# Kernel optimization log

Hardware: AMD Instinct MI355X
Metric: run time of the kernel (lower is better)

## Reference

```python
import jax, jax.numpy as jnp
import numpy as np

NUM_HEADS = 8
NUM_GROUPS = 32
EPS = 1e-5


def group_norm(x, gamma, beta):
    b, c, h, w = x.shape
    xg = x.reshape(b, NUM_GROUPS, c // NUM_GROUPS, h, w)
    mean = jnp.mean(xg, axis=(2, 3, 4), keepdims=True)
    var = jnp.var(xg, axis=(2, 3, 4), keepdims=True)
    xn = ((xg - mean) * jax.lax.rsqrt(var + EPS)).reshape(b, c, h, w)
    return xn * gamma[None, :, None, None] + beta[None, :, None, None]


def setup_inputs() -> dict:
    key = jax.random.key(0)
    ks = jax.random.split(key, 4)
    b, c, h, w = 16, 512, 32, 32
    x = jax.random.normal(ks[0], (b, c, h, w), dtype=jnp.float32)
    gn_gamma = jnp.ones((c,), dtype=jnp.float32)
    gn_beta = jnp.zeros((c,), dtype=jnp.float32)
    qkv_w = jax.random.normal(ks[1], (3 * c, c), dtype=jnp.float32) * (1.0 / np.sqrt(c))
    qkv_b = jnp.zeros((3 * c,), dtype=jnp.float32)
    proj_w = jax.random.normal(ks[2], (c, c), dtype=jnp.float32) * (1.0 / np.sqrt(c))
    proj_b = jnp.zeros((c,), dtype=jnp.float32)
    return {"x": x, "gn_gamma": gn_gamma, "gn_beta": gn_beta,
            "qkv_w": qkv_w, "qkv_b": qkv_b, "proj_w": proj_w, "proj_b": proj_b}


def reference(x, gn_gamma, gn_beta, qkv_w, qkv_b, proj_w, proj_b):
    b, c, h, w = x.shape
    hd = c // NUM_HEADS
    hw = h * w

    xn = group_norm(x, gn_gamma, gn_beta)
    # 1x1 conv == channel matmul
    qkv = jnp.einsum('oc,bchw->bohw', qkv_w, xn) + qkv_b[None, :, None, None]
    q, k, v = jnp.split(qkv, 3, axis=1)
    q = q.reshape(b, NUM_HEADS, hd, hw)
    k = k.reshape(b, NUM_HEADS, hd, hw)
    v = v.reshape(b, NUM_HEADS, hd, hw)

    scale = 1.0 / np.sqrt(hd)
    attn = jnp.einsum('bhdt,bhds->bhts', q, k) * scale  # [b,H,hw,hw]
    attn = jax.nn.softmax(attn, axis=-1)
    h_attn = jnp.einsum('bhts,bhds->bhdt', attn, v).reshape(b, c, h, w)

    h_attn = jnp.einsum('oc,bchw->bohw', proj_w, h_attn) + proj_b[None, :, None, None]
    return x + h_attn
```

## Files before the change

kernel.cpp:

```cpp
#include <hip/hip_runtime.h>
#include <math.h>

#define NUM_HEADS 8
#define NUM_GROUPS 32
#define EPS 1e-5f

constexpr int B  = 16;
constexpr int C  = 512;
constexpr int HW = 1024;
constexpr int HD = 64;

typedef short bf16x8 __attribute__((ext_vector_type(8)));
typedef float f32x4  __attribute__((ext_vector_type(4)));

#define QSCALE 0.1803368801111f

__device__ inline unsigned short f2bf(float f) {
    union { float f; unsigned int u; } v; v.f = f;
    unsigned int r = (v.u + 0x7FFFu + ((v.u >> 16) & 1u)) >> 16;
    return (unsigned short)r;
}

__device__ __forceinline__ unsigned int pack_trunc(float lo, float hi) {
    return __builtin_amdgcn_perm(__float_as_uint(hi), __float_as_uint(lo), 0x07060302u);
}

__device__ __forceinline__ void gld_lds16(void* lds, const void* g) {
    __builtin_amdgcn_global_load_lds(
        (const __attribute__((address_space(1))) void*)g,
        (__attribute__((address_space(3))) void*)lds, 16, 0, 0);
}

__global__ __launch_bounds__(256)
void groupnorm_t_kernel(const float* __restrict__ x,
                        const float* __restrict__ gamma,
                        const float* __restrict__ beta,
                        unsigned short* __restrict__ xnT) {
    const int bg = blockIdx.x;
    const int b = bg >> 5, g = bg & 31;
    const size_t base = ((size_t)b * C + (size_t)g * 16) * HW;

    float v[4][16];
    float sum = 0.f, sumsq = 0.f;
    #pragma unroll
    for (int p = 0; p < 4; ++p) {
        const int t = threadIdx.x + p * 256;
        #pragma unroll
        for (int cl = 0; cl < 16; ++cl) {
            const float f = x[base + (size_t)cl * HW + t];
            v[p][cl] = f;
            sum += f;
            sumsq += f * f;
        }
    }
    #pragma unroll
    for (int off = 32; off > 0; off >>= 1) {
        sum   += __shfl_down(sum, off, 64);
        sumsq += __shfl_down(sumsq, off, 64);
    }
    __shared__ float s_sum[4], s_sq[4];
    const int wid = threadIdx.x >> 6, lane = threadIdx.x & 63;
    if (lane == 0) { s_sum[wid] = sum; s_sq[wid] = sumsq; }
    __syncthreads();
    const float tsum = s_sum[0] + s_sum[1] + s_sum[2] + s_sum[3];
    const float tsq  = s_sq[0] + s_sq[1] + s_sq[2] + s_sq[3];
    const float mean = tsum * (1.0f / 16384.f);
    const float var  = tsq * (1.0f / 16384.f) - mean * mean;
    const float rstd = rsqrtf(var + EPS);

    float ga[16], be[16];
    #pragma unroll
    for (int cl = 0; cl < 16; ++cl) {
        ga[cl] = gamma[g * 16 + cl] * rstd;
        be[cl] = beta[g * 16 + cl] - mean * ga[cl];
    }

    #pragma unroll
    for (int p = 0; p < 4; ++p) {
        const int t = threadIdx.x + p * 256;
        unsigned short pk[16];
        #pragma unroll
        for (int cl = 0; cl < 16; ++cl)
            pk[cl] = f2bf(v[p][cl] * ga[cl] + be[cl]);
        unsigned short* dst = xnT + ((size_t)(b * 1024 + t)) * 512 + g * 16;
        *(uint4*)dst = *(const uint4*)pk;
        *(uint4*)(dst + 8) = *(const uint4*)(pk + 8);
    }
}

__global__ __launch_bounds__(256)
void wconv_kernel(const float* __restrict__ qkv_w,
                  const float* __restrict__ proj_w,
                  unsigned short* __restrict__ wqb) {
    const int i = blockIdx.x * 256 + threadIdx.x;
    const int n1 = 786432 / 4;
    const int nt = 1048576 / 4;
    if (i >= nt) return;
    const float4 v = (i < n1) ? ((const float4*)qkv_w)[i]
                              : ((const float4*)proj_w)[i - n1];
    ushort4 r;
    r.x = f2bf(v.x); r.y = f2bf(v.y); r.z = f2bf(v.z); r.w = f2bf(v.w);
    ((ushort4*)wqb)[i] = r;
}

__device__ __forceinline__ void mfma_gemm_core(const char* __restrict__ Ab,
                                               const char* __restrict__ Bb,
                                               unsigned short* As,
                                               unsigned short* Bs,
                                               f32x4 acc[4][4]) {
    const int tid = threadIdx.x;
    const int w = tid >> 6, lane = tid & 63;
    const int lo = lane & 15, q4 = lane >> 4;
    const int wm = w >> 1, wn = w & 1;
    const int lrow = lane >> 2, lkc = lane & 3;

    for (int k0 = 0; k0 < 512; k0 += 32) {
        __syncthreads();
        #pragma unroll
        for (int i = 0; i < 2; ++i) {
            const int row = w * 32 + i * 16 + lrow;
            const int kc = lkc ^ ((row >> 1) & 3);
            const size_t goff = (size_t)row * 1024 + k0 * 2 + kc * 16;
            gld_lds16((char*)As + w * 2048 + i * 1024, Ab + goff);
            gld_lds16((char*)Bs + w * 2048 + i * 1024, Bb + goff);
        }
        __syncthreads();

        bf16x8 af[4], bfr[4];
        #pragma unroll
        for (int i = 0; i < 4; ++i) {
            const int ra = wm * 64 + i * 16 + lo;
            af[i]  = *(const bf16x8*)(As + ra * 32 + (q4 ^ ((ra >> 1) & 3)) * 8);
            const int rb = wn * 64 + i * 16 + lo;
            bfr[i] = *(const bf16x8*)(Bs + rb * 32 + (q4 ^ ((rb >> 1) & 3)) * 8);
        }
        #pragma unroll
        for (int mi = 0; mi < 4; ++mi)
            #pragma unroll
            for (int ni = 0; ni < 4; ++ni)
                acc[mi][ni] = __builtin_amdgcn_mfma_f32_16x16x32_bf16(
                    af[mi], bfr[ni], acc[mi][ni], 0, 0, 0);
    }
}

__global__ __launch_bounds__(256)
void qkv_mfma_kernel(const unsigned short* __restrict__ wqb,
                     const unsigned short* __restrict__ xnT,
                     const float* __restrict__ qkv_b,
                     unsigned short* __restrict__ Qt,
                     unsigned short* __restrict__ Kt,
                     unsigned short* __restrict__ Vb) {
    __shared__ __align__(16) unsigned short SMEM[8192];
    unsigned short* As = SMEM;
    unsigned short* Bs = SMEM + 4096;
    const int batch = blockIdx.z;
    const int mBase = blockIdx.y * 128, nBase = blockIdx.x * 128;

    f32x4 acc[4][4] = {};
    mfma_gemm_core((const char*)(wqb + (size_t)mBase * 512),
                   (const char*)(xnT + ((size_t)batch * 1024 + nBase) * 512),
                   As, Bs, acc);

    const int tid = threadIdx.x;
    const int w = tid >> 6, lane = tid & 63;
    const int lo = lane & 15, q4 = lane >> 4;
    const int wm = w >> 1, wn = w & 1;
    const int mw = mBase + wm * 64;
    const int tb = nBase + wn * 64;

    __syncthreads();

    if (mw < 1024) {
        const bool isQ = mw < 512;
        const int head = (mw >> 6) & 7;
        unsigned short* dst = (isQ ? Qt : Kt) + (((size_t)batch * 8 + head) << 16);
        const float sc = isQ ? QSCALE : 1.0f;
        #pragma unroll
        for (int mi = 0; mi < 4; ++mi) {
            const float4 bq = *(const float4*)(qkv_b + mw + mi * 16 + q4 * 4);
            #pragma unroll
            for (int ni = 0; ni < 4; ++ni) {
                const int t = tb + ni * 16 + lo;
                ushort4 pk;
                pk.x = f2bf((acc[mi][ni][0] + bq.x) * sc);
                pk.y = f2bf((acc[mi][ni][1] + bq.y) * sc);
                pk.z = f2bf((acc[mi][ni][2] + bq.z) * sc);
                pk.w = f2bf((acc[mi][ni][3] + bq.w) * sc);
                *(ushort4*)(dst + (size_t)t * 64 + mi * 16 + q4 * 4) = pk;
            }
        }
    } else {
        unsigned short* T = SMEM + w * 2048;
        unsigned short* Vrow = Vb + (size_t)batch * 524288 + (size_t)(mw - 1024) * 1024 + tb;
        const int rl8 = lane >> 3, c8 = lane & 7;
        #pragma unroll
        for (int p = 0; p < 2; ++p) {
            #pragma unroll
            for (int mi2 = 0; mi2 < 2; ++mi2) {
                const int mi = 2 * p + mi2;
                const float4 bq = *(const float4*)(qkv_b + mw + mi * 16 + q4 * 4);
                const int dl = mi2 * 16 + q4 * 4;
                #pragma unroll
                for (int ni = 0; ni < 4; ++ni) {
                    const int tl = ni * 16 + lo;
                    T[(dl + 0) * 64 + tl] = f2bf(acc[mi][ni][0] + bq.x);
                    T[(dl + 1) * 64 + tl] = f2bf(acc[mi][ni][1] + bq.y);
                    T[(dl + 2) * 64 + tl] = f2bf(acc[mi][ni][2] + bq.z);
                    T[(dl + 3) * 64 + tl] = f2bf(acc[mi][ni][3] + bq.w);
                }
            }
            #pragma unroll
            for (int i = 0; i < 4; ++i) {
                const int dl = i * 8 + rl8;
                const uint4 val = *(const uint4*)&T[dl * 64 + c8 * 8];
                *(uint4*)(Vrow + (size_t)(p * 32 + dl) * 1024 + c8 * 8) = val;
            }
        }
    }
}

__global__ __launch_bounds__(256, 2)
void attn_mfma_kernel(const unsigned short* __restrict__ Qt,
                      const unsigned short* __restrict__ Kt,
                      const unsigned short* __restrict__ Vb,
                      unsigned short* __restrict__ attnT) {
    const int bh = blockIdx.x;
    const int b = bh >> 3, h = bh & 7;
    const int tBase = blockIdx.y * 256;
    const int tid = threadIdx.x;
    const int w = tid >> 6, lane = tid & 63;
    const int lo = lane & 15, q4 = lane >> 4;
    const int xr = lo & 7;

    __shared__ __align__(16) unsigned short Ks[2][64 * 64];
    __shared__ __align__(16) unsigned short Vs[2][64 * 64];
    __shared__ __align__(16) unsigned short Ps[4][64 * 64];

    const unsigned short* Kp = Kt + ((size_t)bh << 16);
    const unsigned short* Vp = Vb + ((size_t)b * 512 + h * 64) * 1024;

    bf16x8 qf[4][2];
    {
        const unsigned short* Qp = Qt + ((size_t)bh * 1024 + tBase + 64 * w) * 64;
        #pragma unroll
        for (int nt = 0; nt < 4; ++nt) {
            qf[nt][0] = *(const bf16x8*)(Qp + (size_t)(16 * nt + lo) * 64 + 8 * q4);
            qf[nt][1] = *(const bf16x8*)(Qp + (size_t)(16 * nt + lo) * 64 + 32 + 8 * q4);
        }
    }

    const int rl = lane >> 3, p8 = lane & 7;
    auto stage = [&](unsigned short* Kd, unsigned short* Vd, int s0) {
        #pragma unroll
        for (int cc = 0; cc < 2; ++cc) {
            const int r = 16 * w + 8 * cc + rl;
            const int j = p8 ^ (r & 7);
            gld_lds16(Kd + (16 * w + 8 * cc) * 64, Kp + (size_t)(s0 + r) * 64 + j * 8);
            gld_lds16(Vd + (16 * w + 8 * cc) * 64, Vp + (size_t)r * 1024 + s0 + j * 8);
        }
    };

    f32x4 oacc[4][4] = {};
    float lrun[4] = {0.f, 0.f, 0.f, 0.f};
    unsigned short* Pw = Ps[w];

    stage(Ks[0], Vs[0], 0);

    for (int i = 0; i < 16; ++i) {
        __syncthreads();
        if (i < 15) stage(Ks[(i + 1) & 1], Vs[(i + 1) & 1], (i + 1) * 64);
        const unsigned short* Kcur = Ks[i & 1];
        const unsigned short* Vcur = Vs[i & 1];

        f32x4 sacc[4][4] = {};
        #pragma unroll
        for (int mt = 0; mt < 4; ++mt) {
            const unsigned short* kr = Kcur + (16 * mt + lo) * 64;
            const bf16x8 a0 = *(const bf16x8*)(kr + ((q4    ) ^ xr) * 8);
            const bf16x8 a1 = *(const bf16x8*)(kr + ((q4 + 4) ^ xr) * 8);
            #pragma unroll
            for (int nt = 0; nt < 4; ++nt) {
                sacc[mt][nt] = __builtin_amdgcn_mfma_f32_16x16x32_bf16(a0, qf[nt][0], sacc[mt][nt], 0, 0, 0);
                sacc[mt][nt] = __builtin_amdgcn_mfma_f32_16x16x32_bf16(a1, qf[nt][1], sacc[mt][nt], 0, 0, 0);
            }
        }

        #pragma unroll
        for (int nt = 0; nt < 4; ++nt) {
            float ps = 0.f;
            const int t = 16 * nt + lo;
            #pragma unroll
            for (int mt = 0; mt < 4; ++mt) {
                const f32x4 s = sacc[mt][nt];
                const float p0 = exp2f(s[0]);
                const float p1 = exp2f(s[1]);
                const float p2 = exp2f(s[2]);
                const float p3 = exp2f(s[3]);
                ps += (p0 + p1) + (p2 + p3);
                uint2 pk;
                pk.x = pack_trunc(p0, p1);
                pk.y = pack_trunc(p2, p3);
                const int sc = 2 * mt + (q4 >> 1);
                *(uint2*)(Pw + t * 64 + ((sc ^ xr) * 8) + 4 * (q4 & 1)) = pk;
            }
            lrun[nt] += ps;
        }

        bf16x8 bp[4][2];
        #pragma unroll
        for (int nt = 0; nt < 4; ++nt) {
            const unsigned short* pr = Pw + (16 * nt + lo) * 64;
            bp[nt][0] = *(const bf16x8*)(pr + ((q4    ) ^ xr) * 8);
            bp[nt][1] = *(const bf16x8*)(pr + ((q4 + 4) ^ xr) * 8);
        }
        #pragma unroll
        for (int mt = 0; mt < 4; ++mt) {
            const unsigned short* vr = Vcur + (16 * mt + lo) * 64;
            const bf16x8 v0 = *(const bf16x8*)(vr + ((q4    ) ^ xr) * 8);
            const bf16x8 v1 = *(const bf16x8*)(vr + ((q4 + 4) ^ xr) * 8);
            #pragma unroll
            for (int nt = 0; nt < 4; ++nt) {
                oacc[mt][nt] = __builtin_amdgcn_mfma_f32_16x16x32_bf16(v0, bp[nt][0], oacc[mt][nt], 0, 0, 0);
                oacc[mt][nt] = __builtin_amdgcn_mfma_f32_16x16x32_bf16(v1, bp[nt][1], oacc[mt][nt], 0, 0, 0);
            }
        }
    }

    #pragma unroll
    for (int nt = 0; nt < 4; ++nt) {
        float lt = lrun[nt];
        lt += __shfl_xor(lt, 16, 64);
        lt += __shfl_xor(lt, 32, 64);
        const float inv = 1.0f / lt;
        const int t = tBase + 64 * w + 16 * nt + lo;
        unsigned short* op = attnT + ((size_t)(b * 1024 + t)) * 512 + h * 64;
        #pragma unroll
        for (int mt = 0; mt < 4; ++mt) {
            uint2 pk;
            pk.x = pack_trunc(oacc[mt][nt][0] * inv, oacc[mt][nt][1] * inv);
            pk.y = pack_trunc(oacc[mt][nt][2] * inv, oacc[mt][nt][3] * inv);
            *(uint2*)(op + 16 * mt + 4 * q4) = pk;
        }
    }
}

__global__ __launch_bounds__(256)
void proj_mfma_kernel(const unsigned short* __restrict__ wpb,
                      const unsigned short* __restrict__ attnT,
                      const float* __restrict__ proj_b,
                      const float* __restrict__ x,
                      float* __restrict__ out) {
    __shared__ __align__(16) unsigned short As[128 * 32];
    __shared__ __align__(16) unsigned short Bs[128 * 32];
    const int batch = blockIdx.z;
    const int mBase = blockIdx.y * 128, nBase = blockIdx.x * 128;

    f32x4 acc[4][4] = {};
    mfma_gemm_core((const char*)(wpb + (size_t)mBase * 512),
                   (const char*)(attnT + ((size_t)batch * 1024 + nBase) * 512),
                   As, Bs, acc);

    const int tid = threadIdx.x;
    const int w = tid >> 6, lane = tid & 63;
    const int lo = lane & 15, q4 = lane >> 4;
    const int wm = w >> 1, wn = w & 1;
    const float* xb = x + (size_t)batch * 524288;
    float* ob = out + (size_t)batch * 524288;

    #pragma unroll
    for (int mi = 0; mi < 4; ++mi) {
        const int m0 = mBase + wm * 64 + mi * 16 + q4 * 4;
        const float4 bq = *(const float4*)(proj_b + m0);
        #pragma unroll
        for (int ni = 0; ni < 4; ++ni) {
            const int t = nBase + wn * 64 + ni * 16 + lo;
            const size_t o0 = (size_t)m0 * 1024 + t;
            ob[o0]          = acc[mi][ni][0] + bq.x + xb[o0];
            ob[o0 + 1024]   = acc[mi][ni][1] + bq.y + xb[o0 + 1024];
            ob[o0 + 2048]   = acc[mi][ni][2] + bq.z + xb[o0 + 2048];
            ob[o0 + 3072]   = acc[mi][ni][3] + bq.w + xb[o0 + 3072];
        }
    }
}

extern "C" void kernel_launch(void* const* d_in, const int* in_sizes, int n_in,
                              void* d_out, int out_size, void* d_ws, size_t ws_size,
                              hipStream_t stream) {
    const float* x        = (const float*)d_in[0];
    const float* gn_gamma = (const float*)d_in[1];
    const float* gn_beta  = (const float*)d_in[2];
    const float* qkv_w    = (const float*)d_in[3];
    const float* qkv_b    = (const float*)d_in[4];
    const float* proj_w   = (const float*)d_in[5];
    const float* proj_b   = (const float*)d_in[6];
    float* out = (float*)d_out;

    char* wsc = (char*)d_ws;
    unsigned short* xnT   = (unsigned short*)(wsc);
    unsigned short* Qt    = (unsigned short*)(wsc + 16777216);
    unsigned short* Kt    = (unsigned short*)(wsc + 33554432);
    unsigned short* Vb    = (unsigned short*)(wsc + 50331648);
    unsigned short* attnT = (unsigned short*)(wsc + 67108864);
    unsigned short* wqb   = (unsigned short*)(wsc + 83886080);
    unsigned short* wpb   = wqb + 786432;

    groupnorm_t_kernel<<<B * NUM_GROUPS, 256, 0, stream>>>(x, gn_gamma, gn_beta, xnT);

    wconv_kernel<<<1024, 256, 0, stream>>>(qkv_w, proj_w, wqb);

    {
        dim3 grid(HW / 128, (3 * C) / 128, B);
        qkv_mfma_kernel<<<grid, 256, 0, stream>>>(wqb, xnT, qkv_b, Qt, Kt, Vb);
    }

    {
        dim3 grid(B * NUM_HEADS, HW / 256);
        attn_mfma_kernel<<<grid, 256, 0, stream>>>(Qt, Kt, Vb, attnT);
    }

    {
        dim3 grid(HW / 128, C / 128, B);
        proj_mfma_kernel<<<grid, 256, 0, stream>>>(wpb, attnT, proj_b, x, out);
    }
}
```

Measured before the change: 239.0 us.

## Split attention over key halves with combine kernel and XCD-aware block mapping

The attention kernel now splits the key/value sequence into two halves per block, doubling the grid to 1024 blocks. Blocks are remapped so each XCD handles contiguous heads for L2 reuse. A new combine kernel merges the partial outputs and row sums. The K/V tiles are no longer double buffered, so loads are not overlapped with compute, and the PV multiply is split into two phases to reduce register pressure, allowing three blocks per CU. This adds a bf16 round trip of partial outputs through global memory plus an extra launch.

```diff
diff --git a/kernel.cpp b/kernel.cpp
--- a/kernel.cpp
+++ b/kernel.cpp
@@ -219,22 +219,28 @@
     }
 }
 
-__global__ __launch_bounds__(256, 2)
+__global__ __launch_bounds__(256, 3)
 void attn_mfma_kernel(const unsigned short* __restrict__ Qt,
                       const unsigned short* __restrict__ Kt,
                       const unsigned short* __restrict__ Vb,
-                      unsigned short* __restrict__ attnT) {
-    const int bh = blockIdx.x;
+                      unsigned short* __restrict__ Opart,
+                      float* __restrict__ lpart) {
+    const int blk = blockIdx.x;
+    const int cxd = blk & 7, j = blk >> 3;
+    const int bh = cxd * 16 + (j >> 3);
+    const int ts = j & 7;
+    const int tt = ts >> 1, sh = ts & 1;
     const int b = bh >> 3, h = bh & 7;
-    const int tBase = blockIdx.y * 256;
+    const int tBase = tt * 256;
+    const int sBase = sh * 512;
     const int tid = threadIdx.x;
     const int w = tid >> 6, lane = tid & 63;
     const int lo = lane & 15, q4 = lane >> 4;
     const int xr = lo & 7;
 
-    __shared__ __align__(16) unsigned short Ks[2][64 * 64];
-    __shared__ __align__(16) unsigned short Vs[2][64 * 64];
-    __shared__ __align__(16) unsigned short Ps[4][64 * 64];
+    __shared__ __align__(16) unsigned short Ks[64 * 64];
+    __shared__ __align__(16) unsigned short Vs[64 * 64];
+    __shared__ __align__(16) unsigned short Ps[4 * 4096];
 
     const unsigned short* Kp = Kt + ((size_t)bh << 16);
     const unsigned short* Vp = Vb + ((size_t)b * 512 + h * 64) * 1024;
@@ -250,98 +256,119 @@
     }
 
     const int rl = lane >> 3, p8 = lane & 7;
-    auto stage = [&](unsigned short* Kd, unsigned short* Vd, int s0) {
+    auto stage = [&](int s0) {
         #pragma unroll
         for (int cc = 0; cc < 2; ++cc) {
             const int r = 16 * w + 8 * cc + rl;
-            const int j = p8 ^ (r & 7);
-            gld_lds16(Kd + (16 * w + 8 * cc) * 64, Kp + (size_t)(s0 + r) * 64 + j * 8);
-            gld_lds16(Vd + (16 * w + 8 * cc) * 64, Vp + (size_t)r * 1024 + s0 + j * 8);
+            const int jj = p8 ^ (r & 7);
+            gld_lds16(Ks + (16 * w + 8 * cc) * 64, Kp + (size_t)(s0 + r) * 64 + jj * 8);
+            gld_lds16(Vs + (16 * w + 8 * cc) * 64, Vp + (size_t)r * 1024 + s0 + jj * 8);
         }
     };
 
     f32x4 oacc[4][4] = {};
     float lrun[4] = {0.f, 0.f, 0.f, 0.f};
-    unsigned short* Pw = Ps[w];
-
-    stage(Ks[0], Vs[0], 0);
-
-    for (int i = 0; i < 16; ++i) {
+    unsigned short* Pw = Ps + w * 4096;
+
+    for (int i = 0; i < 8; ++i) {
+        if (i) __syncthreads();
+        stage(sBase + i * 64);
         __syncthreads();
-        if (i < 15) stage(Ks[(i + 1) & 1], Vs[(i + 1) & 1], (i + 1) * 64);
-        const unsigned short* Kcur = Ks[i & 1];
-        const unsigned short* Vcur = Vs[i & 1];
-
-        f32x4 sacc[4][4] = {};
-        #pragma unroll
-        for (int mt = 0; mt < 4; ++mt) {
-            const unsigned short* kr = Kcur + (16 * mt + lo) * 64;
-            const bf16x8 a0 = *(const bf16x8*)(kr + ((q4    ) ^ xr) * 8);
-            const bf16x8 a1 = *(const bf16x8*)(kr + ((q4 + 4) ^ xr) * 8);
+        #pragma unroll
+        for (int ph = 0; ph < 2; ++ph) {
+            f32x4 sacc[2][4] = {};
+            #pragma unroll
+            for (int ml = 0; ml < 2; ++ml) {
+                const unsigned short* kr = Ks + (16 * (2 * ph + ml) + lo) * 64;
+                const bf16x8 a0 = *(const bf16x8*)(kr + ((q4    ) ^ xr) * 8);
+                const bf16x8 a1 = *(const bf16x8*)(kr + ((q4 + 4) ^ xr) * 8);
+                #pragma unroll
+                for (int nt = 0; nt < 4; ++nt) {
+                    sacc[ml][nt] = __builtin_amdgcn_mfma_f32_16x16x32_bf16(a0, qf[nt][0], sacc[ml][nt], 0, 0, 0);
+                    sacc[ml][nt] = __builtin_amdgcn_mfma_f32_16x16x32_bf16(a1, qf[nt][1], sacc[ml][nt], 0, 0, 0);
+                }
+            }
             #pragma unroll
             for (int nt = 0; nt < 4; ++nt) {
-                sacc[mt][nt] = __builtin_amdgcn_mfma_f32_16x16x32_bf16(a0, qf[nt][0], sacc[mt][nt], 0, 0, 0);
-                sacc[mt][nt] = __builtin_amdgcn_mfma_f32_16x16x32_bf16(a1, qf[nt][1], sacc[mt][nt], 0, 0, 0);
-            }
-        }
-
-        #pragma unroll
-        for (int nt = 0; nt < 4; ++nt) {
-            float ps = 0.f;
-            const int t = 16 * nt + lo;
-            #pragma unroll
-            for (int mt = 0; mt < 4; ++mt) {
-                const f32x4 s = sacc[mt][nt];
-                const float p0 = exp2f(s[0]);
-                const float p1 = exp2f(s[1]);
-                const float p2 = exp2f(s[2]);
-                const float p3 = exp2f(s[3]);
-                ps += (p0 + p1) + (p2 + p3);
-                uint2 pk;
-                pk.x = pack_trunc(p0, p1);
-                pk.y = pack_trunc(p2, p3);
-                const int sc = 2 * mt + (q4 >> 1);
-                *(uint2*)(Pw + t * 64 + ((sc ^ xr) * 8) + 4 * (q4 & 1)) = pk;
-            }
-            lrun[nt] += ps;
-        }
-
-        bf16x8 bp[4][2];
-        #pragma unroll
-        for (int nt = 0; nt < 4; ++nt) {
-            const unsigned short* pr = Pw + (16 * nt + lo) * 64;
-            bp[nt][0] = *(const bf16x8*)(pr + ((q4    ) ^ xr) * 8);
-            bp[nt][1] = *(const bf16x8*)(pr + ((q4 + 4) ^ xr) * 8);
-        }
-        #pragma unroll
-        for (int mt = 0; mt < 4; ++mt) {
-            const unsigned short* vr = Vcur + (16 * mt + lo) * 64;
-            const bf16x8 v0 = *(const bf16x8*)(vr + ((q4    ) ^ xr) * 8);
-            const bf16x8 v1 = *(const bf16x8*)(vr + ((q4 + 4) ^ xr) * 8);
-            #pragma unroll
-            for (int nt = 0; nt < 4; ++nt) {
-                oacc[mt][nt] = __builtin_amdgcn_mfma_f32_16x16x32_bf16(v0, bp[nt][0], oacc[mt][nt], 0, 0, 0);
-                oacc[mt][nt] = __builtin_amdgcn_mfma_f32_16x16x32_bf16(v1, bp[nt][1], oacc[mt][nt], 0, 0, 0);
-            }
-        }
-    }
-
+                const int t = 16 * nt + lo;
+                float ps = 0.f;
+                #pragma unroll
+                for (int ml = 0; ml < 2; ++ml) {
+                    const f32x4 s = sacc[ml][nt];
+                    const float p0 = exp2f(s[0]);
+                    const float p1 = exp2f(s[1]);
+                    const float p2 = exp2f(s[2]);
+                    const float p3 = exp2f(s[3]);
+                    ps += (p0 + p1) + (p2 + p3);
+                    uint2 pk;
+                    pk.x = pack_trunc(p0, p1);
+                    pk.y = pack_trunc(p2, p3);
+                    const int sc = 4 * ph + 2 * ml + (q4 >> 1);
+                    *(uint2*)(Pw + t * 64 + ((sc ^ xr) * 8) + 4 * (q4 & 1)) = pk;
+                }
+                lrun[nt] += ps;
+            }
+            bf16x8 bp[4];
+            #pragma unroll
+            for (int nt = 0; nt < 4; ++nt)
+                bp[nt] = *(const bf16x8*)(Pw + (16 * nt + lo) * 64 + (((q4 + 4 * ph) ^ xr) * 8));
+            #pragma unroll
+            for (int md = 0; md < 4; ++md) {
+                const bf16x8 av = *(const bf16x8*)(Vs + (16 * md + lo) * 64 + (((q4 + 4 * ph) ^ xr) * 8));
+                #pragma unroll
+                for (int nt = 0; nt < 4; ++nt)
+                    oacc[md][nt] = __builtin_amdgcn_mfma_f32_16x16x32_bf16(av, bp[nt], oacc[md][nt], 0, 0, 0);
+            }
+        }
+    }
+
+    const size_t tw = (size_t)tBase + 64 * w;
+    const size_t pbase = ((size_t)sh * 128 + bh) * 1024;
     #pragma unroll
     for (int nt = 0; nt < 4; ++nt) {
         float lt = lrun[nt];
         lt += __shfl_xor(lt, 16, 64);
         lt += __shfl_xor(lt, 32, 64);
-        const float inv = 1.0f / lt;
-        const int t = tBase + 64 * w + 16 * nt + lo;
-        unsigned short* op = attnT + ((size_t)(b * 1024 + t)) * 512 + h * 64;
-        #pragma unroll
-        for (int mt = 0; mt < 4; ++mt) {
+        const int tl = 16 * nt + lo;
+        if (q4 == 0) lpart[pbase + tw + tl] = lt;
+        unsigned short* op = Opart + (pbase + tw + tl) * 64;
+        #pragma unroll
+        for (int md = 0; md < 4; ++md) {
             uint2 pk;
-            pk.x = pack_trunc(oacc[mt][nt][0] * inv, oacc[mt][nt][1] * inv);
-            pk.y = pack_trunc(oacc[mt][nt][2] * inv, oacc[mt][nt][3] * inv);
-            *(uint2*)(op + 16 * mt + 4 * q4) = pk;
-        }
-    }
+            pk.x = pack_trunc(oacc[md][nt][0], oacc[md][nt][1]);
+            pk.y = pack_trunc(oacc[md][nt][2], oacc[md][nt][3]);
+            *(uint2*)(op + 16 * md + 4 * q4) = pk;
+        }
+    }
+}
+
+__global__ __launch_bounds__(256)
+void attn_combine_kernel(const unsigned short* __restrict__ Opart,
+                         const float* __restrict__ lpart,
+                         unsigned short* __restrict__ attnT) {
+    const int idx = blockIdx.x * 256 + threadIdx.x;
+    const int d8 = idx & 7;
+    const int t  = (idx >> 3) & 1023;
+    const int bh = idx >> 13;
+    const int b = bh >> 3, h = bh & 7;
+    const size_t po = ((size_t)bh * 1024 + t) * 64 + d8 * 8;
+    const uint4 o0 = *(const uint4*)(Opart + po);
+    const uint4 o1 = *(const uint4*)(Opart + ((size_t)128 * 1024 * 64) + po);
+    const float l0 = lpart[(size_t)bh * 1024 + t];
+    const float l1 = lpart[(size_t)128 * 1024 + (size_t)bh * 1024 + t];
+    const float inv = 1.0f / (l0 + l1);
+    const unsigned int* a = (const unsigned int*)&o0;
+    const unsigned int* c = (const unsigned int*)&o1;
+    unsigned int outv[4];
+    #pragma unroll
+    for (int k = 0; k < 4; ++k) {
+        const float alo = __uint_as_float(a[k] << 16);
+        const float ahi = __uint_as_float(a[k] & 0xFFFF0000u);
+        const float blo = __uint_as_float(c[k] << 16);
+        const float bhi = __uint_as_float(c[k] & 0xFFFF0000u);
+        outv[k] = pack_trunc((alo + blo) * inv, (ahi + bhi) * inv);
+    }
+    *(uint4*)(attnT + ((size_t)(b * 1024 + t)) * 512 + h * 64 + d8 * 8) = *(uint4*)outv;
 }
 
 __global__ __launch_bounds__(256)
@@ -403,6 +430,8 @@
     unsigned short* attnT = (unsigned short*)(wsc + 67108864);
     unsigned short* wqb   = (unsigned short*)(wsc + 83886080);
     unsigned short* wpb   = wqb + 786432;
+    unsigned short* Opart = (unsigned short*)(wsc + 88080384);
+    float*          lpart = (float*)(wsc + 121634816);
 
     groupnorm_t_kernel<<<B * NUM_GROUPS, 256, 0, stream>>>(x, gn_gamma, gn_beta, xnT);
 
@@ -413,10 +442,9 @@
         qkv_mfma_kernel<<<grid, 256, 0, stream>>>(wqb, xnT, qkv_b, Qt, Kt, Vb);
     }
 
-    {
-        dim3 grid(B * NUM_HEADS, HW / 256);
-        attn_mfma_kernel<<<grid, 256, 0, stream>>>(Qt, Kt, Vb, attnT);
-    }
+    attn_mfma_kernel<<<1024, 256, 0, stream>>>(Qt, Kt, Vb, Opart, lpart);
+
+    attn_combine_kernel<<<4096, 256, 0, stream>>>(Opart, lpart, attnT);
 
     {
         dim3 grid(HW / 128, C / 128, B);
```

After: 336.3 us. +40.7%, slower.

## Halve attention query tile and drop K/V double buffering for higher occupancy

Applied to the files above, without the earlier changes.

Each attention block now handles 128 query rows instead of 256 (32 per wave), doubling the grid to 1024 blocks. K/V staging becomes single-buffered, with a sync before and after each load, and the per-wave P buffer shrinks. Launch bounds rise to 4 blocks per SM to allow more resident waves and fewer registers per thread. In exchange, K/V tiles are re-read twice as often and global-load latency is no longer overlapped by double buffering within a block.

```diff
diff --git a/kernel.cpp b/kernel.cpp
--- a/kernel.cpp
+++ b/kernel.cpp
@@ -219,76 +219,73 @@
     }
 }
 
-__global__ __launch_bounds__(256, 2)
+__global__ __launch_bounds__(256, 4)
 void attn_mfma_kernel(const unsigned short* __restrict__ Qt,
                       const unsigned short* __restrict__ Kt,
                       const unsigned short* __restrict__ Vb,
                       unsigned short* __restrict__ attnT) {
     const int bh = blockIdx.x;
     const int b = bh >> 3, h = bh & 7;
-    const int tBase = blockIdx.y * 256;
+    const int tBase = blockIdx.y * 128;
     const int tid = threadIdx.x;
     const int w = tid >> 6, lane = tid & 63;
     const int lo = lane & 15, q4 = lane >> 4;
     const int xr = lo & 7;
 
-    __shared__ __align__(16) unsigned short Ks[2][64 * 64];
-    __shared__ __align__(16) unsigned short Vs[2][64 * 64];
-    __shared__ __align__(16) unsigned short Ps[4][64 * 64];
+    __shared__ __align__(16) unsigned short Ks[64 * 64];
+    __shared__ __align__(16) unsigned short Vs[64 * 64];
+    __shared__ __align__(16) unsigned short Ps[4 * 2048];
 
     const unsigned short* Kp = Kt + ((size_t)bh << 16);
     const unsigned short* Vp = Vb + ((size_t)b * 512 + h * 64) * 1024;
 
-    bf16x8 qf[4][2];
+    bf16x8 qf[2][2];
     {
-        const unsigned short* Qp = Qt + ((size_t)bh * 1024 + tBase + 64 * w) * 64;
-        #pragma unroll
-        for (int nt = 0; nt < 4; ++nt) {
+        const unsigned short* Qp = Qt + ((size_t)bh * 1024 + tBase + 32 * w) * 64;
+        #pragma unroll
+        for (int nt = 0; nt < 2; ++nt) {
             qf[nt][0] = *(const bf16x8*)(Qp + (size_t)(16 * nt + lo) * 64 + 8 * q4);
             qf[nt][1] = *(const bf16x8*)(Qp + (size_t)(16 * nt + lo) * 64 + 32 + 8 * q4);
         }
     }
 
     const int rl = lane >> 3, p8 = lane & 7;
-    auto stage = [&](unsigned short* Kd, unsigned short* Vd, int s0) {
+    auto stage = [&](int s0) {
         #pragma unroll
         for (int cc = 0; cc < 2; ++cc) {
             const int r = 16 * w + 8 * cc + rl;
-            const int j = p8 ^ (r & 7);
-            gld_lds16(Kd + (16 * w + 8 * cc) * 64, Kp + (size_t)(s0 + r) * 64 + j * 8);
-            gld_lds16(Vd + (16 * w + 8 * cc) * 64, Vp + (size_t)r * 1024 + s0 + j * 8);
+            const int jj = p8 ^ (r & 7);
+            gld_lds16(Ks + (16 * w + 8 * cc) * 64, Kp + (size_t)(s0 + r) * 64 + jj * 8);
+            gld_lds16(Vs + (16 * w + 8 * cc) * 64, Vp + (size_t)r * 1024 + s0 + jj * 8);
         }
     };
 
-    f32x4 oacc[4][4] = {};
-    float lrun[4] = {0.f, 0.f, 0.f, 0.f};
-    unsigned short* Pw = Ps[w];
-
-    stage(Ks[0], Vs[0], 0);
+    f32x4 oacc[4][2] = {};
+    float lrun[2] = {0.f, 0.f};
+    unsigned short* Pw = Ps + w * 2048;
 
     for (int i = 0; i < 16; ++i) {
+        if (i) __syncthreads();
+        stage(i * 64);
         __syncthreads();
-        if (i < 15) stage(Ks[(i + 1) & 1], Vs[(i + 1) & 1], (i + 1) * 64);
-        const unsigned short* Kcur = Ks[i & 1];
-        const unsigned short* Vcur = Vs[i & 1];
-
-        f32x4 sacc[4][4] = {};
+
+        f32x4 sacc[4][2] = {};
         #pragma unroll
         for (int mt = 0; mt < 4; ++mt) {
-            const unsigned short* kr = Kcur + (16 * mt + lo) * 64;
+            const unsigned short* kr = Ks + (16 * mt + lo) * 64;
             const bf16x8 a0 = *(const bf16x8*)(kr + ((q4    ) ^ xr) * 8);
             const bf16x8 a1 = *(const bf16x8*)(kr + ((q4 + 4) ^ xr) * 8);
             #pragma unroll
-            for (int nt = 0; nt < 4; ++nt) {
+            for (int nt = 0; nt < 2; ++nt) {
                 sacc[mt][nt] = __builtin_amdgcn_mfma_f32_16x16x32_bf16(a0, qf[nt][0], sacc[mt][nt], 0, 0, 0);
                 sacc[mt][nt] = __builtin_amdgcn_mfma_f32_16x16x32_bf16(a1, qf[nt][1], sacc[mt][nt], 0, 0, 0);
             }
         }
 
         #pragma unroll
-        for (int nt = 0; nt < 4; ++nt) {
+        for (int nt = 0; nt < 2; ++nt) {
+            const int t = 16 * nt + lo;
             float ps = 0.f;
-            const int t = 16 * nt + lo;
             #pragma unroll
             for (int mt = 0; mt < 4; ++mt) {
                 const f32x4 s = sacc[mt][nt];
@@ -306,40 +303,40 @@
             lrun[nt] += ps;
         }
 
-        bf16x8 bp[4][2];
-        #pragma unroll
-        for (int nt = 0; nt < 4; ++nt) {
+        bf16x8 bp[2][2];
+        #pragma unroll
+        for (int nt = 0; nt < 2; ++nt) {
             const unsigned short* pr = Pw + (16 * nt + lo) * 64;
             bp[nt][0] = *(const bf16x8*)(pr + ((q4    ) ^ xr) * 8);
             bp[nt][1] = *(const bf16x8*)(pr + ((q4 + 4) ^ xr) * 8);
         }
         #pragma unroll
-        for (int mt = 0; mt < 4; ++mt) {
-            const unsigned short* vr = Vcur + (16 * mt + lo) * 64;
+        for (int md = 0; md < 4; ++md) {
+            const unsigned short* vr = Vs + (16 * md + lo) * 64;
             const bf16x8 v0 = *(const bf16x8*)(vr + ((q4    ) ^ xr) * 8);
             const bf16x8 v1 = *(const bf16x8*)(vr + ((q4 + 4) ^ xr) * 8);
             #pragma unroll
-            for (int nt = 0; nt < 4; ++nt) {
-                oacc[mt][nt] = __builtin_amdgcn_mfma_f32_16x16x32_bf16(v0, bp[nt][0], oacc[mt][nt], 0, 0, 0);
-                oacc[mt][nt] = __builtin_amdgcn_mfma_f32_16x16x32_bf16(v1, bp[nt][1], oacc[mt][nt], 0, 0, 0);
-            }
-        }
-    }
-
-    #pragma unroll
-    for (int nt = 0; nt < 4; ++nt) {
+            for (int nt = 0; nt < 2; ++nt) {
+                oacc[md][nt] = __builtin_amdgcn_mfma_f32_16x16x32_bf16(v0, bp[nt][0], oacc[md][nt], 0, 0, 0);
+                oacc[md][nt] = __builtin_amdgcn_mfma_f32_16x16x32_bf16(v1, bp[nt][1], oacc[md][nt], 0, 0, 0);
+            }
+        }
+    }
+
+    #pragma unroll
+    for (int nt = 0; nt < 2; ++nt) {
         float lt = lrun[nt];
         lt += __shfl_xor(lt, 16, 64);
         lt += __shfl_xor(lt, 32, 64);
         const float inv = 1.0f / lt;
-        const int t = tBase + 64 * w + 16 * nt + lo;
+        const int t = tBase + 32 * w + 16 * nt + lo;
         unsigned short* op = attnT + ((size_t)(b * 1024 + t)) * 512 + h * 64;
         #pragma unroll
-        for (int mt = 0; mt < 4; ++mt) {
+        for (int md = 0; md < 4; ++md) {
             uint2 pk;
-            pk.x = pack_trunc(oacc[mt][nt][0] * inv, oacc[mt][nt][1] * inv);
-            pk.y = pack_trunc(oacc[mt][nt][2] * inv, oacc[mt][nt][3] * inv);
-            *(uint2*)(op + 16 * mt + 4 * q4) = pk;
+            pk.x = pack_trunc(oacc[md][nt][0] * inv, oacc[md][nt][1] * inv);
+            pk.y = pack_trunc(oacc[md][nt][2] * inv, oacc[md][nt][3] * inv);
+            *(uint2*)(op + 16 * md + 4 * q4) = pk;
         }
     }
 }
@@ -414,7 +411,7 @@
     }
 
     {
-        dim3 grid(B * NUM_HEADS, HW / 256);
+        dim3 grid(B * NUM_HEADS, HW / 128);
         attn_mfma_kernel<<<grid, 256, 0, stream>>>(Qt, Kt, Vb, attnT);
     }
 
```

Result: faster. 222.2 us (-7.0%).
